# Optimization experiments

Hardware: AMD Instinct MI355X
Metric: run time of the kernel (lower is better)

The kernel has to match this reference:

```python
import jax, jax.numpy as jnp
import numpy as np

S, B, D, H, V, MF = 50, 128, 512, 512, 30000, 32
PAD = 0


def setup_inputs() -> dict:
    key = jax.random.key(0)
    ks = jax.random.split(key, 10)
    inp = {
        "user": jax.random.normal(ks[0], (B, MF), dtype=jnp.float32),
        "item": jax.random.normal(ks[1], (B, MF), dtype=jnp.float32),
        "review_input": jax.random.randint(ks[2], (S, B), 0, V, dtype=jnp.int64),
        "review_target": jax.random.randint(ks[3], (S, B), 0, V, dtype=jnp.int64),
        # learned parameters
        "word_emb": jax.random.normal(ks[4], (V, D), dtype=jnp.float32) * 0.02,
        "W_ih": jax.random.normal(ks[5], (3 * H, D), dtype=jnp.float32) * (1.0 / np.sqrt(D)),
        "W_hh": jax.random.normal(ks[6], (3 * H, H), dtype=jnp.float32) * (1.0 / np.sqrt(H)),
        "b_ih": jnp.zeros((3 * H,), dtype=jnp.float32),
        "b_hh": jnp.zeros((3 * H,), dtype=jnp.float32),
        "W_out": jax.random.normal(ks[7], (V, H), dtype=jnp.float32) * (1.0 / np.sqrt(H)),
        "b_out": jnp.zeros((V,), dtype=jnp.float32),
    }
    return inp


def _gru_forward(review_input, word_emb, W_ih, W_hh, b_ih, b_hh, W_out, b_out, batch):
    Hdim = W_hh.shape[1]
    h0 = jnp.zeros((batch, Hdim), dtype=word_emb.dtype)  # encoder returns zeros
    x = word_emb[review_input]  # [S, B, D] embedding lookup (dropout is identity in eval)

    def step(h, x_t):
        gi = x_t @ W_ih.T + b_ih            # [B, 3H]
        gh = h @ W_hh.T + b_hh              # [B, 3H]
        i_r, i_z, i_n = jnp.split(gi, 3, axis=-1)
        h_r, h_z, h_n = jnp.split(gh, 3, axis=-1)
        r = jax.nn.sigmoid(i_r + h_r)
        z = jax.nn.sigmoid(i_z + h_z)
        n = jnp.tanh(i_n + r * h_n)
        h_new = (1.0 - z) * n + z * h
        return h_new, h_new

    _, hs = jax.lax.scan(step, h0, x)       # [S, B, H]
    logits = jnp.einsum('sbh,vh->sbv', hs, W_out) + b_out  # decode from hidden_state
    return logits.reshape(-1, W_out.shape[0])  # [S*B, V], same row order as torch.cat


def reference(user, item, review_input, review_target, word_emb, W_ih, W_hh,
              b_ih, b_hh, W_out, b_out):
    batch = user.shape[0]
    logits = _gru_forward(review_input, word_emb, W_ih, W_hh, b_ih, b_hh,
                          W_out, b_out, batch)
    targets = review_target.reshape(-1)                     # [S*B]
    logp = jax.nn.log_softmax(logits, axis=-1)
    nll = -jnp.take_along_axis(logp, targets[:, None], axis=-1)[:, 0]
    mask = (targets != PAD)
    out_loss = jnp.where(mask, nll, 0.0)                    # reduction='none', ignore_index=PAD
    denom = jnp.maximum(jnp.sum(mask.astype(logits.dtype)), 1.0)
    obj = jnp.sum(out_loss) / denom                         # mean over non-pad tokens
    return (out_loss, obj)
```

## Files before the change

kernel.cpp:

```cpp
#include <hip/hip_runtime.h>
#include <hip/hip_bf16.h>

typedef __attribute__((ext_vector_type(8))) short short8;
typedef __attribute__((ext_vector_type(4))) float floatx4;

#define S_LEN  50
#define BATCH  128
#define DIM    512
#define HID    512
#define G3     1536
#define VOCAB  30000
#define TOKENS 6400
#define NB256  118
#define NVC    472
#define NWG    (25 * NB256)

__device__ __forceinline__ float bf2f(short u) {
    union { unsigned int i; float f; } c;
    c.i = ((unsigned int)(unsigned short)u) << 16;
    return c.f;
}
__device__ __forceinline__ unsigned short f2bf(float x) {
    __hip_bfloat16 h = __float2bfloat16(x);
    unsigned short u;
    __builtin_memcpy(&u, &h, 2);
    return u;
}

__global__ void k_cvt_bf16(const float* __restrict__ src,
                           unsigned short* __restrict__ dst, int n8) {
    int g = blockIdx.x * 256 + threadIdx.x;
    if (g >= n8) return;
    const float* s = src + (size_t)g * 8;
    union { short8 v; unsigned short u[8]; } o;
#pragma unroll
    for (int i = 0; i < 8; ++i) o.u[i] = f2bf(s[i]);
    *(short8*)(dst + (size_t)g * 8) = o.v;
}

__global__ void k_gather_x(const float* __restrict__ emb, const int* __restrict__ idx,
                           unsigned short* __restrict__ X) {
    int g = blockIdx.x * 256 + threadIdx.x;
    int token = g >> 6;
    int chunk = (g & 63) << 3;
    const float* src = emb + (size_t)idx[token] * DIM + chunk;
    union { short8 v; unsigned short u[8]; } o;
#pragma unroll
    for (int i = 0; i < 8; ++i) o.u[i] = f2bf(src[i]);
    *(short8*)(X + (size_t)token * DIM + chunk) = o.v;
}

__launch_bounds__(256)
__global__ void k_gemm_gi(const unsigned short* __restrict__ X,
                          const unsigned short* __restrict__ Wih,
                          const float* __restrict__ b_ih,
                          float* __restrict__ GI) {
    __shared__ unsigned short As[64][72];
    __shared__ unsigned short Bs[64][72];
    int m0 = blockIdx.x * 64;
    int n0 = blockIdx.y * 64;
    int t = threadIdx.x;
    int w = t >> 6, lane = t & 63;
    floatx4 zero = {0.f, 0.f, 0.f, 0.f};
    floatx4 acc[4];
#pragma unroll
    for (int i = 0; i < 4; ++i) acc[i] = zero;
    int srow = t >> 2, scol = (t & 3) * 16;
    for (int k0 = 0; k0 < DIM; k0 += 64) {
        *(short8*)&As[srow][scol]     = *(const short8*)(X   + (size_t)(m0 + srow) * DIM + k0 + scol);
        *(short8*)&As[srow][scol + 8] = *(const short8*)(X   + (size_t)(m0 + srow) * DIM + k0 + scol + 8);
        *(short8*)&Bs[srow][scol]     = *(const short8*)(Wih + (size_t)(n0 + srow) * DIM + k0 + scol);
        *(short8*)&Bs[srow][scol + 8] = *(const short8*)(Wih + (size_t)(n0 + srow) * DIM + k0 + scol + 8);
        __syncthreads();
#pragma unroll
        for (int kt = 0; kt < 2; ++kt) {
            short8 a = *(const short8*)&As[w * 16 + (lane & 15)][kt * 32 + (lane >> 4) * 8];
#pragma unroll
            for (int nt = 0; nt < 4; ++nt) {
                short8 b = *(const short8*)&Bs[nt * 16 + (lane & 15)][kt * 32 + (lane >> 4) * 8];
                acc[nt] = __builtin_amdgcn_mfma_f32_16x16x32_bf16(a, b, acc[nt], 0, 0, 0);
            }
        }
        __syncthreads();
    }
#pragma unroll
    for (int nt = 0; nt < 4; ++nt)
#pragma unroll
        for (int r = 0; r < 4; ++r) {
            int row = m0 + w * 16 + (lane >> 4) * 4 + r;
            int col = n0 + nt * 16 + (lane & 15);
            GI[(size_t)row * G3 + col] = acc[nt][r] + b_ih[col];
        }
}

__launch_bounds__(64)
__global__ void k_gru_step(const float* __restrict__ GI,
                           const unsigned short* __restrict__ Whh,
                           const float* __restrict__ b_hh,
                           float* __restrict__ hf,
                           const unsigned short* __restrict__ hin,
                           unsigned short* __restrict__ hout,
                           int s) {
    int lane = threadIdx.x & 63;
    int bg = blockIdx.x & 7;
    int hs = blockIdx.x >> 3;
    int jc = hs * 16 + (lane & 15);

    const unsigned short* pa  = hin + (size_t)(bg * 16 + (lane & 15)) * HID + (lane >> 4) * 8;
    const unsigned short* pb0 = Whh + (size_t)(0 * HID + jc) * DIM + (lane >> 4) * 8;
    const unsigned short* pb1 = Whh + (size_t)(1 * HID + jc) * DIM + (lane >> 4) * 8;
    const unsigned short* pb2 = Whh + (size_t)(2 * HID + jc) * DIM + (lane >> 4) * 8;

    floatx4 acc0 = {0.f, 0.f, 0.f, 0.f};
    floatx4 acc1 = {0.f, 0.f, 0.f, 0.f};
    floatx4 acc2 = {0.f, 0.f, 0.f, 0.f};
#pragma unroll
    for (int kt = 0; kt < 16; ++kt) {
        short8 a = *(const short8*)(pa + kt * 32);
        acc0 = __builtin_amdgcn_mfma_f32_16x16x32_bf16(a, *(const short8*)(pb0 + kt * 32), acc0, 0, 0, 0);
        acc1 = __builtin_amdgcn_mfma_f32_16x16x32_bf16(a, *(const short8*)(pb1 + kt * 32), acc1, 0, 0, 0);
        acc2 = __builtin_amdgcn_mfma_f32_16x16x32_bf16(a, *(const short8*)(pb2 + kt * 32), acc2, 0, 0, 0);
    }
    float bhr = b_hh[jc], bhz = b_hh[jc + 512], bhn = b_hh[jc + 1024];
#pragma unroll
    for (int r = 0; r < 4; ++r) {
        int brow = bg * 16 + (lane >> 4) * 4 + r;
        int tok = s * BATCH + brow;
        const float* gi = GI + (size_t)tok * G3;
        float rg = 1.f / (1.f + __expf(-(gi[jc] + acc0[r] + bhr)));
        float zg = 1.f / (1.f + __expf(-(gi[jc + 512] + acc1[r] + bhz)));
        float ng = tanhf(gi[jc + 1024] + rg * (acc2[r] + bhn));
        size_t hidx = (size_t)brow * HID + jc;
        float hn = (1.f - zg) * ng + zg * hf[hidx];
        hf[hidx] = hn;
        hout[hidx] = f2bf(hn);
    }
}

__launch_bounds__(1024, 4)
__global__ void k_decode(const unsigned short* __restrict__ HS,
                         const unsigned short* __restrict__ Wout,
                         const float* __restrict__ b_out,
                         float* __restrict__ partial) {
    __shared__ unsigned short As[2][256 * 64];
    __shared__ unsigned short Bs[2][256 * 64];

    int bid = blockIdx.x;
    int xcd = bid & 7, pos = bid >> 3;
    int p = (xcd < 6 ? xcd * 369 : 2214 + (xcd - 6) * 368) + pos;
    int sgrp = p / 200;
    int rr   = p - sgrp * 200;
    int mb, nb;
    if (sgrp < 14) { mb = rr >> 3; nb = sgrp * 8 + (rr & 7); }
    else           { int q6 = rr / 6; mb = q6; nb = 112 + (rr - q6 * 6); }
    int m0 = mb * 256, n0 = nb * 256;

    int t = threadIdx.x, w = t >> 6, lane = t & 63;
    int wr = w >> 2, wc = w & 3;

    floatx4 zero = {0.f, 0.f, 0.f, 0.f};
    floatx4 acc[4][4];
#pragma unroll
    for (int mi = 0; mi < 4; ++mi)
#pragma unroll
        for (int ni = 0; ni < 4; ++ni) acc[mi][ni] = zero;

    int srow = t >> 2;
    int scb  = (t & 3) * 32;
    int swz  = (srow & 7) << 4;
    const unsigned short* gA = HS + (size_t)(m0 + srow) * DIM + (t & 3) * 16;
    int vrow = n0 + srow; if (vrow > VOCAB - 1) vrow = VOCAB - 1;
    const unsigned short* gB = Wout + (size_t)vrow * DIM + (t & 3) * 16;
    int wo0 = (srow * 128 + scb)      ^ swz;
    int wo1 = (srow * 128 + scb + 16) ^ swz;

    int roA[4][2], roB[4][2];
#pragma unroll
    for (int mi = 0; mi < 4; ++mi)
#pragma unroll
        for (int kt = 0; kt < 2; ++kt) {
            int row = wr * 64 + mi * 16 + (lane & 15);
            roA[mi][kt] = (row * 128 + kt * 64 + (lane >> 4) * 16) ^ ((row & 7) << 4);
        }
#pragma unroll
    for (int ni = 0; ni < 4; ++ni)
#pragma unroll
        for (int kt = 0; kt < 2; ++kt) {
            int row = wc * 64 + ni * 16 + (lane & 15);
            roB[ni][kt] = (row * 128 + kt * 64 + (lane >> 4) * 16) ^ ((row & 7) << 4);
        }

    {
        short8 a0 = *(const short8*)(gA);
        short8 a1 = *(const short8*)(gA + 8);
        short8 b0 = *(const short8*)(gB);
        short8 b1 = *(const short8*)(gB + 8);
        *(short8*)((char*)As[0] + wo0) = a0;
        *(short8*)((char*)As[0] + wo1) = a1;
        *(short8*)((char*)Bs[0] + wo0) = b0;
        *(short8*)((char*)Bs[0] + wo1) = b1;
    }
    __syncthreads();

    for (int ki = 0; ki < 8; ++ki) {
        int cur = ki & 1;
        short8 a0, a1, b0, b1;
        if (ki < 7) {
            int k0 = (ki + 1) * 64;
            a0 = *(const short8*)(gA + k0);
            a1 = *(const short8*)(gA + k0 + 8);
            b0 = *(const short8*)(gB + k0);
            b1 = *(const short8*)(gB + k0 + 8);
        }
#pragma unroll
        for (int kt = 0; kt < 2; ++kt) {
            short8 af[4], bf[4];
#pragma unroll
            for (int mi = 0; mi < 4; ++mi)
                af[mi] = *(const short8*)((const char*)As[cur] + roA[mi][kt]);
#pragma unroll
            for (int ni = 0; ni < 4; ++ni)
                bf[ni] = *(const short8*)((const char*)Bs[cur] + roB[ni][kt]);
#pragma unroll
            for (int mi = 0; mi < 4; ++mi)
#pragma unroll
                for (int ni = 0; ni < 4; ++ni)
                    acc[mi][ni] = __builtin_amdgcn_mfma_f32_16x16x32_bf16(af[mi], bf[ni], acc[mi][ni], 0, 0, 0);
        }
        if (ki < 7) {
            int nxt = cur ^ 1;
            *(short8*)((char*)As[nxt] + wo0) = a0;
            *(short8*)((char*)As[nxt] + wo1) = a1;
            *(short8*)((char*)Bs[nxt] + wo0) = b0;
            *(short8*)((char*)Bs[nxt] + wo1) = b1;
        }
        __syncthreads();
    }

    float esum[4][4];
#pragma unroll
    for (int mi = 0; mi < 4; ++mi)
#pragma unroll
        for (int r = 0; r < 4; ++r) esum[mi][r] = 0.f;
#pragma unroll
    for (int ni = 0; ni < 4; ++ni) {
        int v = n0 + wc * 64 + ni * 16 + (lane & 15);
        bool ok = v < VOCAB;
        float bo = ok ? b_out[v] : 0.f;
#pragma unroll
        for (int mi = 0; mi < 4; ++mi)
#pragma unroll
            for (int r = 0; r < 4; ++r) {
                float logit = acc[mi][ni][r] + bo;
                esum[mi][r] += ok ? __expf(logit) : 0.f;
            }
    }
#pragma unroll
    for (int d = 1; d < 16; d <<= 1)
#pragma unroll
        for (int mi = 0; mi < 4; ++mi)
#pragma unroll
            for (int r = 0; r < 4; ++r) esum[mi][r] += __shfl_xor(esum[mi][r], d, 64);
    if ((lane & 15) == 0) {
#pragma unroll
        for (int mi = 0; mi < 4; ++mi)
#pragma unroll
            for (int r = 0; r < 4; ++r) {
                int tok = m0 + wr * 64 + mi * 16 + (lane >> 4) * 4 + r;
                partial[(size_t)tok * 512 + nb * 4 + wc] = esum[mi][r];
            }
    }
}

__global__ void k_reduce_lse(const float* __restrict__ partial, float* __restrict__ lse) {
    int tok = blockIdx.x * 4 + (threadIdx.x >> 6);
    int lane = threadIdx.x & 63;
    float s = 0.f;
    for (int j = lane; j < NVC; j += 64) s += partial[(size_t)tok * 512 + j];
#pragma unroll
    for (int d = 1; d < 64; d <<= 1) s += __shfl_xor(s, d, 64);
    if (lane == 0) lse[tok] = logf(s);
}

__global__ void k_tlogit(const unsigned short* __restrict__ HS,
                         const unsigned short* __restrict__ Wout,
                         const float* __restrict__ b_out,
                         const int* __restrict__ target,
                         float* __restrict__ tlg) {
    int tok = blockIdx.x * 4 + (threadIdx.x >> 6);
    int lane = threadIdx.x & 63;
    int tg = target[tok];
    short8 a = *(const short8*)(HS + (size_t)tok * DIM + lane * 8);
    short8 b = *(const short8*)(Wout + (size_t)tg * DIM + lane * 8);
    float s = 0.f;
#pragma unroll
    for (int i = 0; i < 8; ++i) s += bf2f(a[i]) * bf2f(b[i]);
#pragma unroll
    for (int d = 1; d < 64; d <<= 1) s += __shfl_xor(s, d, 64);
    if (lane == 0) tlg[tok] = s + b_out[tg];
}

__global__ void k_finalize(const float* __restrict__ lse, const float* __restrict__ tlg,
                           const int* __restrict__ target, float* __restrict__ out) {
    __shared__ float ssum[256];
    __shared__ float scnt[256];
    int t = threadIdx.x;
    float ls = 0.f, lc = 0.f;
    for (int i = t; i < TOKENS; i += 256) {
        int tg = target[i];
        float loss = (tg != 0) ? (lse[i] - tlg[i]) : 0.f;
        out[i] = loss;
        ls += loss;
        lc += (tg != 0) ? 1.f : 0.f;
    }
    ssum[t] = ls; scnt[t] = lc;
    __syncthreads();
    for (int d = 128; d > 0; d >>= 1) {
        if (t < d) { ssum[t] += ssum[t + d]; scnt[t] += scnt[t + d]; }
        __syncthreads();
    }
    if (t == 0) out[TOKENS] = ssum[0] / fmaxf(scnt[0], 1.f);
}

extern "C" void kernel_launch(void* const* d_in, const int* in_sizes, int n_in,
                              void* d_out, int out_size, void* d_ws, size_t ws_size,
                              hipStream_t stream) {
    const int*   review_input  = (const int*)d_in[2];
    const int*   review_target = (const int*)d_in[3];
    const float* word_emb      = (const float*)d_in[4];
    const float* W_ih          = (const float*)d_in[5];
    const float* W_hh          = (const float*)d_in[6];
    const float* b_ih          = (const float*)d_in[7];
    const float* b_hh          = (const float*)d_in[8];
    const float* W_out         = (const float*)d_in[9];
    const float* b_out         = (const float*)d_in[10];
    float* out = (float*)d_out;

    char* ws = (char*)d_ws;
    size_t off = 0;
    auto alloc = [&](size_t n) { char* p = ws + off; off += (n + 255) & ~(size_t)255; return p; };
    unsigned short* Xb    = (unsigned short*)alloc((size_t)TOKENS * DIM * 2);
    unsigned short* Wihb  = (unsigned short*)alloc((size_t)G3 * DIM * 2);
    unsigned short* Whhb  = (unsigned short*)alloc((size_t)G3 * HID * 2);
    unsigned short* Woutb = (unsigned short*)alloc((size_t)VOCAB * DIM * 2);
    unsigned short* HS    = (unsigned short*)alloc((size_t)TOKENS * HID * 2);
    unsigned short* hzero = (unsigned short*)alloc((size_t)BATCH * HID * 2);
    float* hf      = (float*)alloc((size_t)BATCH * HID * 4);
    float* GI      = (float*)alloc((size_t)TOKENS * G3 * 4);
    float* partial = (float*)alloc((size_t)TOKENS * 512 * 4);
    float* lse     = (float*)alloc((size_t)TOKENS * 4);
    float* tlg     = (float*)alloc((size_t)TOKENS * 4);
    (void)ws_size; (void)in_sizes; (void)n_in; (void)out_size;

    k_cvt_bf16<<<dim3((G3 * DIM / 8 + 255) / 256), dim3(256), 0, stream>>>(W_ih, Wihb, G3 * DIM / 8);
    k_cvt_bf16<<<dim3((G3 * HID / 8 + 255) / 256), dim3(256), 0, stream>>>(W_hh, Whhb, G3 * HID / 8);
    k_cvt_bf16<<<dim3((VOCAB * DIM / 8 + 255) / 256), dim3(256), 0, stream>>>(W_out, Woutb, VOCAB * DIM / 8);
    k_gather_x<<<dim3(TOKENS * DIM / 8 / 256), dim3(256), 0, stream>>>(word_emb, review_input, Xb);

    k_gemm_gi<<<dim3(TOKENS / 64, G3 / 64), dim3(256), 0, stream>>>(Xb, Wihb, b_ih, GI);

    hipMemsetAsync(hf, 0, (size_t)BATCH * HID * 4, stream);
    hipMemsetAsync(hzero, 0, (size_t)BATCH * HID * 2, stream);
    for (int s = 0; s < S_LEN; ++s) {
        const unsigned short* hin = s ? (HS + (size_t)(s - 1) * BATCH * HID) : hzero;
        unsigned short* hout = HS + (size_t)s * BATCH * HID;
        k_gru_step<<<dim3(256), dim3(64), 0, stream>>>(GI, Whhb, b_hh, hf, hin, hout, s);
    }

    k_decode<<<dim3(NWG), dim3(1024), 0, stream>>>(HS, Woutb, b_out, partial);
    k_reduce_lse<<<dim3(TOKENS / 4), dim3(256), 0, stream>>>(partial, lse);
    k_tlogit<<<dim3(TOKENS / 4), dim3(256), 0, stream>>>(HS, Woutb, b_out, review_target, tlg);
    k_finalize<<<dim3(1), dim3(256), 0, stream>>>(lse, tlg, review_target, out);
}
```

Before: 530.9 us.

## Fuse prep kernels, retile input GEMM to 128x128, skip zero-state matmul

Merges the three weight-conversion launches and the embedding gather into one kernel. Retiles the input-gate GEMM to 128x128 blocks with XOR-swizzled shared memory and a grouped block order for more reuse and fewer bank conflicts. The first GRU step now skips the hidden-state matmul because the state is zero, which also removes the zero buffer and its memset. The LSE reduction and target-logit kernels are merged into one launch. Together these cut launch overhead and improve GEMM efficiency, at the cost of more registers per thread in the larger tile.

```diff
diff --git a/kernel.cpp b/kernel.cpp
--- a/kernel.cpp
+++ b/kernel.cpp
@@ -15,6 +15,12 @@
 #define NVC    472
 #define NWG    (25 * NB256)
 
+#define N8_WIH   (G3 * DIM / 8)
+#define N8_WHH   (G3 * HID / 8)
+#define N8_WOUT  (VOCAB * DIM / 8)
+#define N8_GATH  (TOKENS * DIM / 8)
+#define N8_TOTAL (N8_WIH + N8_WHH + N8_WOUT + N8_GATH)
+
 __device__ __forceinline__ float bf2f(short u) {
     union { unsigned int i; float f; } c;
     c.i = ((unsigned int)(unsigned short)u) << 16;
@@ -27,27 +33,33 @@
     return u;
 }
 
-__global__ void k_cvt_bf16(const float* __restrict__ src,
-                           unsigned short* __restrict__ dst, int n8) {
+__global__ void k_prep(const float* __restrict__ Wih, const float* __restrict__ Whh,
+                       const float* __restrict__ Wout, const float* __restrict__ emb,
+                       const int* __restrict__ idx,
+                       unsigned short* __restrict__ WihB, unsigned short* __restrict__ WhhB,
+                       unsigned short* __restrict__ WoutB, unsigned short* __restrict__ X) {
     int g = blockIdx.x * 256 + threadIdx.x;
-    if (g >= n8) return;
-    const float* s = src + (size_t)g * 8;
+    const float* src;
+    unsigned short* dst;
+    if (g < N8_WIH) {
+        src = Wih + (size_t)g * 8;  dst = WihB + (size_t)g * 8;
+    } else if (g < N8_WIH + N8_WHH) {
+        int h = g - N8_WIH;
+        src = Whh + (size_t)h * 8;  dst = WhhB + (size_t)h * 8;
+    } else if (g < N8_WIH + N8_WHH + N8_WOUT) {
+        int h = g - (N8_WIH + N8_WHH);
+        src = Wout + (size_t)h * 8; dst = WoutB + (size_t)h * 8;
+    } else {
+        int h = g - (N8_WIH + N8_WHH + N8_WOUT);
+        int token = h >> 6;
+        int chunk = (h & 63) << 3;
+        src = emb + (size_t)idx[token] * DIM + chunk;
+        dst = X + (size_t)token * DIM + chunk;
+    }
     union { short8 v; unsigned short u[8]; } o;
 #pragma unroll
-    for (int i = 0; i < 8; ++i) o.u[i] = f2bf(s[i]);
-    *(short8*)(dst + (size_t)g * 8) = o.v;
-}
-
-__global__ void k_gather_x(const float* __restrict__ emb, const int* __restrict__ idx,
-                           unsigned short* __restrict__ X) {
-    int g = blockIdx.x * 256 + threadIdx.x;
-    int token = g >> 6;
-    int chunk = (g & 63) << 3;
-    const float* src = emb + (size_t)idx[token] * DIM + chunk;
-    union { short8 v; unsigned short u[8]; } o;
-#pragma unroll
     for (int i = 0; i < 8; ++i) o.u[i] = f2bf(src[i]);
-    *(short8*)(X + (size_t)token * DIM + chunk) = o.v;
+    *(short8*)dst = o.v;
 }
 
 __launch_bounds__(256)
@@ -55,41 +67,73 @@
                           const unsigned short* __restrict__ Wih,
                           const float* __restrict__ b_ih,
                           float* __restrict__ GI) {
-    __shared__ unsigned short As[64][72];
-    __shared__ unsigned short Bs[64][72];
-    int m0 = blockIdx.x * 64;
-    int n0 = blockIdx.y * 64;
-    int t = threadIdx.x;
-    int w = t >> 6, lane = t & 63;
+    __shared__ unsigned short As[128 * 64];
+    __shared__ unsigned short Bs[128 * 64];
+    int bid = blockIdx.x;
+    int wgid = (bid % 8) * 75 + bid / 8;
+    int mb = wgid % 50, nb = wgid / 50;
+    int m0 = mb * 128, n0 = nb * 128;
+
+    int t = threadIdx.x, w = t >> 6, lane = t & 63;
+    int wr = w >> 1, wc = w & 1;
+
     floatx4 zero = {0.f, 0.f, 0.f, 0.f};
-    floatx4 acc[4];
-#pragma unroll
-    for (int i = 0; i < 4; ++i) acc[i] = zero;
-    int srow = t >> 2, scol = (t & 3) * 16;
+    floatx4 acc[4][4];
+#pragma unroll
+    for (int mi = 0; mi < 4; ++mi)
+#pragma unroll
+        for (int ni = 0; ni < 4; ++ni) acc[mi][ni] = zero;
+
+    int srow = t >> 1;
+    int scq  = (t & 1) * 32;
+    const unsigned short* gA = X   + (size_t)(m0 + srow) * DIM + scq;
+    const unsigned short* gB = Wih + (size_t)(n0 + srow) * DIM + scq;
+    int wo[4];
+#pragma unroll
+    for (int q = 0; q < 4; ++q)
+        wo[q] = (srow * 128 + scq * 2 + q * 16) ^ ((srow & 7) << 4);
+
     for (int k0 = 0; k0 < DIM; k0 += 64) {
-        *(short8*)&As[srow][scol]     = *(const short8*)(X   + (size_t)(m0 + srow) * DIM + k0 + scol);
-        *(short8*)&As[srow][scol + 8] = *(const short8*)(X   + (size_t)(m0 + srow) * DIM + k0 + scol + 8);
-        *(short8*)&Bs[srow][scol]     = *(const short8*)(Wih + (size_t)(n0 + srow) * DIM + k0 + scol);
-        *(short8*)&Bs[srow][scol + 8] = *(const short8*)(Wih + (size_t)(n0 + srow) * DIM + k0 + scol + 8);
+#pragma unroll
+        for (int q = 0; q < 4; ++q) {
+            *(short8*)((char*)As + wo[q]) = *(const short8*)(gA + k0 + q * 8);
+            *(short8*)((char*)Bs + wo[q]) = *(const short8*)(gB + k0 + q * 8);
+        }
         __syncthreads();
 #pragma unroll
         for (int kt = 0; kt < 2; ++kt) {
-            short8 a = *(const short8*)&As[w * 16 + (lane & 15)][kt * 32 + (lane >> 4) * 8];
-#pragma unroll
-            for (int nt = 0; nt < 4; ++nt) {
-                short8 b = *(const short8*)&Bs[nt * 16 + (lane & 15)][kt * 32 + (lane >> 4) * 8];
-                acc[nt] = __builtin_amdgcn_mfma_f32_16x16x32_bf16(a, b, acc[nt], 0, 0, 0);
+            short8 af[4], bf[4];
+#pragma unroll
+            for (int mi = 0; mi < 4; ++mi) {
+                int row = wr * 64 + mi * 16 + (lane & 15);
+                int off = (row * 128 + kt * 64 + (lane >> 4) * 16) ^ ((row & 7) << 4);
+                af[mi] = *(const short8*)((const char*)As + off);
             }
+#pragma unroll
+            for (int ni = 0; ni < 4; ++ni) {
+                int row = wc * 64 + ni * 16 + (lane & 15);
+                int off = (row * 128 + kt * 64 + (lane >> 4) * 16) ^ ((row & 7) << 4);
+                bf[ni] = *(const short8*)((const char*)Bs + off);
+            }
+#pragma unroll
+            for (int mi = 0; mi < 4; ++mi)
+#pragma unroll
+                for (int ni = 0; ni < 4; ++ni)
+                    acc[mi][ni] = __builtin_amdgcn_mfma_f32_16x16x32_bf16(af[mi], bf[ni], acc[mi][ni], 0, 0, 0);
         }
         __syncthreads();
     }
 #pragma unroll
-    for (int nt = 0; nt < 4; ++nt)
-#pragma unroll
-        for (int r = 0; r < 4; ++r) {
-            int row = m0 + w * 16 + (lane >> 4) * 4 + r;
-            int col = n0 + nt * 16 + (lane & 15);
-            GI[(size_t)row * G3 + col] = acc[nt][r] + b_ih[col];
+    for (int mi = 0; mi < 4; ++mi)
+#pragma unroll
+        for (int ni = 0; ni < 4; ++ni) {
+            int col = n0 + wc * 64 + ni * 16 + (lane & 15);
+            float bo = b_ih[col];
+#pragma unroll
+            for (int r = 0; r < 4; ++r) {
+                int row = m0 + wr * 64 + mi * 16 + (lane >> 4) * 4 + r;
+                GI[(size_t)row * G3 + col] = acc[mi][ni][r] + bo;
+            }
         }
 }
 
@@ -106,20 +150,21 @@
     int hs = blockIdx.x >> 3;
     int jc = hs * 16 + (lane & 15);
 
-    const unsigned short* pa  = hin + (size_t)(bg * 16 + (lane & 15)) * HID + (lane >> 4) * 8;
-    const unsigned short* pb0 = Whh + (size_t)(0 * HID + jc) * DIM + (lane >> 4) * 8;
-    const unsigned short* pb1 = Whh + (size_t)(1 * HID + jc) * DIM + (lane >> 4) * 8;
-    const unsigned short* pb2 = Whh + (size_t)(2 * HID + jc) * DIM + (lane >> 4) * 8;
-
     floatx4 acc0 = {0.f, 0.f, 0.f, 0.f};
     floatx4 acc1 = {0.f, 0.f, 0.f, 0.f};
     floatx4 acc2 = {0.f, 0.f, 0.f, 0.f};
-#pragma unroll
-    for (int kt = 0; kt < 16; ++kt) {
-        short8 a = *(const short8*)(pa + kt * 32);
-        acc0 = __builtin_amdgcn_mfma_f32_16x16x32_bf16(a, *(const short8*)(pb0 + kt * 32), acc0, 0, 0, 0);
-        acc1 = __builtin_amdgcn_mfma_f32_16x16x32_bf16(a, *(const short8*)(pb1 + kt * 32), acc1, 0, 0, 0);
-        acc2 = __builtin_amdgcn_mfma_f32_16x16x32_bf16(a, *(const short8*)(pb2 + kt * 32), acc2, 0, 0, 0);
+    if (s != 0) {
+        const unsigned short* pa  = hin + (size_t)(bg * 16 + (lane & 15)) * HID + (lane >> 4) * 8;
+        const unsigned short* pb0 = Whh + (size_t)(0 * HID + jc) * DIM + (lane >> 4) * 8;
+        const unsigned short* pb1 = Whh + (size_t)(1 * HID + jc) * DIM + (lane >> 4) * 8;
+        const unsigned short* pb2 = Whh + (size_t)(2 * HID + jc) * DIM + (lane >> 4) * 8;
+#pragma unroll
+        for (int kt = 0; kt < 16; ++kt) {
+            short8 a = *(const short8*)(pa + kt * 32);
+            acc0 = __builtin_amdgcn_mfma_f32_16x16x32_bf16(a, *(const short8*)(pb0 + kt * 32), acc0, 0, 0, 0);
+            acc1 = __builtin_amdgcn_mfma_f32_16x16x32_bf16(a, *(const short8*)(pb1 + kt * 32), acc1, 0, 0, 0);
+            acc2 = __builtin_amdgcn_mfma_f32_16x16x32_bf16(a, *(const short8*)(pb2 + kt * 32), acc2, 0, 0, 0);
+        }
     }
     float bhr = b_hh[jc], bhz = b_hh[jc + 512], bhn = b_hh[jc + 1024];
 #pragma unroll
@@ -272,21 +317,12 @@
     }
 }
 
-__global__ void k_reduce_lse(const float* __restrict__ partial, float* __restrict__ lse) {
-    int tok = blockIdx.x * 4 + (threadIdx.x >> 6);
-    int lane = threadIdx.x & 63;
-    float s = 0.f;
-    for (int j = lane; j < NVC; j += 64) s += partial[(size_t)tok * 512 + j];
-#pragma unroll
-    for (int d = 1; d < 64; d <<= 1) s += __shfl_xor(s, d, 64);
-    if (lane == 0) lse[tok] = logf(s);
-}
-
-__global__ void k_tlogit(const unsigned short* __restrict__ HS,
-                         const unsigned short* __restrict__ Wout,
-                         const float* __restrict__ b_out,
-                         const int* __restrict__ target,
-                         float* __restrict__ tlg) {
+__global__ void k_lse_tlg(const float* __restrict__ partial,
+                          const unsigned short* __restrict__ HS,
+                          const unsigned short* __restrict__ Wout,
+                          const float* __restrict__ b_out,
+                          const int* __restrict__ target,
+                          float* __restrict__ lse, float* __restrict__ tlg) {
     int tok = blockIdx.x * 4 + (threadIdx.x >> 6);
     int lane = threadIdx.x & 63;
     int tg = target[tok];
@@ -295,9 +331,17 @@
     float s = 0.f;
 #pragma unroll
     for (int i = 0; i < 8; ++i) s += bf2f(a[i]) * bf2f(b[i]);
-#pragma unroll
-    for (int d = 1; d < 64; d <<= 1) s += __shfl_xor(s, d, 64);
-    if (lane == 0) tlg[tok] = s + b_out[tg];
+    float s2 = 0.f;
+    for (int j = lane; j < NVC; j += 64) s2 += partial[(size_t)tok * 512 + j];
+#pragma unroll
+    for (int d = 1; d < 64; d <<= 1) {
+        s  += __shfl_xor(s, d, 64);
+        s2 += __shfl_xor(s2, d, 64);
+    }
+    if (lane == 0) {
+        tlg[tok] = s + b_out[tg];
+        lse[tok] = logf(s2);
+    }
 }
 
 __global__ void k_finalize(const float* __restrict__ lse, const float* __restrict__ tlg,
@@ -344,7 +388,6 @@
     unsigned short* Whhb  = (unsigned short*)alloc((size_t)G3 * HID * 2);
     unsigned short* Woutb = (unsigned short*)alloc((size_t)VOCAB * DIM * 2);
     unsigned short* HS    = (unsigned short*)alloc((size_t)TOKENS * HID * 2);
-    unsigned short* hzero = (unsigned short*)alloc((size_t)BATCH * HID * 2);
     float* hf      = (float*)alloc((size_t)BATCH * HID * 4);
     float* GI      = (float*)alloc((size_t)TOKENS * G3 * 4);
     float* partial = (float*)alloc((size_t)TOKENS * 512 * 4);
@@ -352,23 +395,19 @@
     float* tlg     = (float*)alloc((size_t)TOKENS * 4);
     (void)ws_size; (void)in_sizes; (void)n_in; (void)out_size;
 
-    k_cvt_bf16<<<dim3((G3 * DIM / 8 + 255) / 256), dim3(256), 0, stream>>>(W_ih, Wihb, G3 * DIM / 8);
-    k_cvt_bf16<<<dim3((G3 * HID / 8 + 255) / 256), dim3(256), 0, stream>>>(W_hh, Whhb, G3 * HID / 8);
-    k_cvt_bf16<<<dim3((VOCAB * DIM / 8 + 255) / 256), dim3(256), 0, stream>>>(W_out, Woutb, VOCAB * DIM / 8);
-    k_gather_x<<<dim3(TOKENS * DIM / 8 / 256), dim3(256), 0, stream>>>(word_emb, review_input, Xb);
-
-    k_gemm_gi<<<dim3(TOKENS / 64, G3 / 64), dim3(256), 0, stream>>>(Xb, Wihb, b_ih, GI);
+    k_prep<<<dim3(N8_TOTAL / 256), dim3(256), 0, stream>>>(
+        W_ih, W_hh, W_out, word_emb, review_input, Wihb, Whhb, Woutb, Xb);
+
+    k_gemm_gi<<<dim3(600), dim3(256), 0, stream>>>(Xb, Wihb, b_ih, GI);
 
     hipMemsetAsync(hf, 0, (size_t)BATCH * HID * 4, stream);
-    hipMemsetAsync(hzero, 0, (size_t)BATCH * HID * 2, stream);
     for (int s = 0; s < S_LEN; ++s) {
-        const unsigned short* hin = s ? (HS + (size_t)(s - 1) * BATCH * HID) : hzero;
+        const unsigned short* hin = s ? (HS + (size_t)(s - 1) * BATCH * HID) : HS;
         unsigned short* hout = HS + (size_t)s * BATCH * HID;
         k_gru_step<<<dim3(256), dim3(64), 0, stream>>>(GI, Whhb, b_hh, hf, hin, hout, s);
     }
 
     k_decode<<<dim3(NWG), dim3(1024), 0, stream>>>(HS, Woutb, b_out, partial);
-    k_reduce_lse<<<dim3(TOKENS / 4), dim3(256), 0, stream>>>(partial, lse);
-    k_tlogit<<<dim3(TOKENS / 4), dim3(256), 0, stream>>>(HS, Woutb, b_out, review_target, tlg);
+    k_lse_tlg<<<dim3(TOKENS / 4), dim3(256), 0, stream>>>(partial, HS, Woutb, b_out, review_target, lse, tlg);
     k_finalize<<<dim3(1), dim3(256), 0, stream>>>(lse, tlg, review_target, out);
 }
```

Result: slower. 565.3 us (+6.5%).
